# Performance work log

Hardware: AMD Instinct MI355X
Metric: run time of the kernel (lower is better)

The kernel has to match this reference:

```python
import jax, jax.numpy as jnp
import numpy as np

HIDDEN = 768
HEADS = 12
HEAD_DIM = HIDDEN // HEADS  # 64


def setup_inputs() -> dict:
    key = jax.random.key(0)
    k1, k2, k3 = jax.random.split(key, 3)
    B, N, C = 64, 197, HIDDEN
    hidden_states = jax.random.normal(k1, (B, N, C), dtype=jnp.float32)
    # qkv Linear: weight [C, 3C] (stored transposed for x @ W), bias [3C]
    w_qkv = jax.random.normal(k2, (C, 3 * C), dtype=jnp.float32) * (1.0 / np.sqrt(C))
    b_qkv = jax.random.normal(k3, (3 * C,), dtype=jnp.float32) * 0.02
    return {"hidden_states": hidden_states, "w_qkv": w_qkv, "b_qkv": b_qkv}


def reference(hidden_states, w_qkv, b_qkv):
    B, N, C = hidden_states.shape
    scale = HEAD_DIM ** -0.5
    qkv = hidden_states @ w_qkv + b_qkv                      # [B, N, 3C]
    qkv = qkv.reshape(B, N, 3, HEADS, HEAD_DIM)
    qkv = jnp.transpose(qkv, (2, 0, 3, 1, 4))                # [3, B, H, N, d]
    q, k, v = qkv[0], qkv[1], qkv[2]
    scores = jnp.einsum("bhqd,bhkd->bhqk", q, k) * scale     # [B, H, N, N]
    probs = jax.nn.softmax(scores, axis=-1)
    # dropout is identity in eval mode (p=0.0)
    ctx = jnp.einsum("bhqk,bhkd->bhqd", probs, v)            # [B, H, N, d]
    ctx = jnp.transpose(ctx, (0, 2, 1, 3)).reshape(B, N, C)  # [B, N, C]
    return ctx
```

## Files before the change

### kernel.cpp

```cpp
#include <hip/hip_runtime.h>

#define M_ROWS 12608
#define K_DIM  768
#define QSZ    9682944
#define XB_ELEMS 9732096

typedef __bf16 bf16x8 __attribute__((ext_vector_type(8)));
typedef float  f32x4  __attribute__((ext_vector_type(4)));

__device__ __forceinline__ unsigned short f2bf(float f) {
    unsigned u = __builtin_bit_cast(unsigned, f);
    u += 0x7fffu + ((u >> 16) & 1u);
    return (unsigned short)(u >> 16);
}

__device__ __forceinline__ void gll16(const unsigned short* g, unsigned short* l) {
    __builtin_amdgcn_global_load_lds(
        (const __attribute__((address_space(1))) unsigned int*)g,
        (__attribute__((address_space(3))) unsigned int*)l, 16, 0, 0);
}

__global__ void x2bf_kernel(const float* __restrict__ X, unsigned short* __restrict__ Xb) {
    size_t base = ((size_t)blockIdx.x * 256 + threadIdx.x) * 8;
    float4 a = *(const float4*)(X + base);
    float4 b = *(const float4*)(X + base + 4);
    ushort4 lo, hi;
    lo.x = f2bf(a.x); lo.y = f2bf(a.y); lo.z = f2bf(a.z); lo.w = f2bf(a.w);
    hi.x = f2bf(b.x); hi.y = f2bf(b.y); hi.z = f2bf(b.z); hi.w = f2bf(b.w);
    *(ushort4*)(Xb + base) = lo;
    *(ushort4*)(Xb + base + 4) = hi;
}

__global__ void wtrans_kernel(const float* __restrict__ W, unsigned short* __restrict__ Wt) {
    __shared__ float tile[32][33];
    int n0 = blockIdx.x * 32, k0 = blockIdx.y * 32;
    int tx = threadIdx.x, ty = threadIdx.y;
#pragma unroll
    for (int i = 0; i < 4; ++i)
        tile[ty + i * 8][tx] = W[(size_t)(k0 + ty + i * 8) * 2304 + n0 + tx];
    __syncthreads();
#pragma unroll
    for (int i = 0; i < 4; ++i)
        Wt[(size_t)(n0 + ty + i * 8) * K_DIM + k0 + tx] = f2bf(tile[tx][ty + i * 8]);
}

__global__ __launch_bounds__(256, 4) void qkv_gemm_kernel(
        const unsigned short* __restrict__ Xb, const unsigned short* __restrict__ Wt,
        const float* __restrict__ bias, unsigned short* __restrict__ qkv) {
    __shared__ __align__(16) unsigned short As[2][4096];
    __shared__ __align__(16) unsigned short Bs[2][4096];

    const int lin = blockIdx.x;
    const int xcd = lin & 7, ix = lin >> 3;
    const int wg = (xcd < 6) ? xcd * 223 + ix : 1338 + (xcd - 6) * 222 + ix;
    const int by = wg / 18, bx = wg - by * 18;
    const int m0 = by * 128, n0 = bx * 128;

    const int t = threadIdx.x;
    const int w = t >> 6, lane = t & 63, quad = lane >> 4, l16 = lane & 15;
    const int wr = (w >> 1) * 64, wc = (w & 1) * 64;

    const int s0 = w * 128 + lane;
    const int r0 = s0 & 127, kc0 = s0 >> 7;
    const int s1 = s0 + 64;
    const int r1 = s1 & 127, kc1 = s1 >> 7;
    const unsigned short* a0 = Xb + (size_t)(m0 + r0) * K_DIM + kc0 * 8;
    const unsigned short* a1 = Xb + (size_t)(m0 + r1) * K_DIM + kc1 * 8;
    const unsigned short* b0 = Wt + (size_t)(n0 + r0) * K_DIM + kc0 * 8;
    const unsigned short* b1 = Wt + (size_t)(n0 + r1) * K_DIM + kc1 * 8;

    f32x4 acc[4][4];
#pragma unroll
    for (int i = 0; i < 4; ++i)
#pragma unroll
        for (int j = 0; j < 4; ++j) acc[i][j] = (f32x4){0.f, 0.f, 0.f, 0.f};

    gll16(a0, &As[0][w * 1024]);
    gll16(a1, &As[0][w * 1024 + 512]);
    gll16(b0, &Bs[0][w * 1024]);
    gll16(b1, &Bs[0][w * 1024 + 512]);
    asm volatile("s_waitcnt vmcnt(0)" ::: "memory");
    __builtin_amdgcn_s_barrier();
    asm volatile("" ::: "memory");

#pragma unroll 2
    for (int kt = 0; kt < 24; ++kt) {
        const int cur = kt & 1, nxt = cur ^ 1;
        const int sk = (kt + 1 < 24 ? kt + 1 : 0) * 32;

        gll16(a0 + sk, &As[nxt][w * 1024]);
        gll16(a1 + sk, &As[nxt][w * 1024 + 512]);
        gll16(b0 + sk, &Bs[nxt][w * 1024]);
        gll16(b1 + sk, &Bs[nxt][w * 1024 + 512]);

        bf16x8 af[4], bfr[4];
#pragma unroll
        for (int i = 0; i < 4; ++i)
            af[i] = *(const bf16x8*)&As[cur][quad * 1024 + (wr + i * 16 + l16) * 8];
#pragma unroll
        for (int j = 0; j < 4; ++j)
            bfr[j] = *(const bf16x8*)&Bs[cur][quad * 1024 + (wc + j * 16 + l16) * 8];

#pragma unroll
        for (int i = 0; i < 4; ++i)
#pragma unroll
            for (int j = 0; j < 4; ++j)
                acc[i][j] = __builtin_amdgcn_mfma_f32_16x16x32_bf16(af[i], bfr[j], acc[i][j], 0, 0, 0);

        asm volatile("s_waitcnt vmcnt(0)" ::: "memory");
        __builtin_amdgcn_s_barrier();
        asm volatile("" ::: "memory");
    }

#pragma unroll
    for (int i = 0; i < 4; ++i) {
#pragma unroll
        for (int j = 0; j < 4; ++j) {
            int gn = n0 + wc + j * 16 + l16;
            int which = gn / 768;
            int rem = gn - which * 768;
            int hh = rem >> 6, dd = rem & 63;
            float bv = bias[gn];
#pragma unroll
            for (int r = 0; r < 4; ++r) {
                int gm = m0 + wr + i * 16 + quad * 4 + r;
                if (gm >= M_ROWS) continue;
                int bb = gm / 197;
                int tok = gm - bb * 197;
                float val = acc[i][j][r] + bv;
                if (which == 0) val *= 0.125f;
                size_t dst = (size_t)which * QSZ +
                             ((size_t)((bb * 12 + hh) * 197 + tok) * 64 + dd);
                qkv[dst] = f2bf(val);
            }
        }
    }
}

__global__ __launch_bounds__(256, 2) void attn_kernel(
        const unsigned short* __restrict__ qkv, float* __restrict__ out) {
    __shared__ __align__(16) unsigned short Ks[197 * 72];
    __shared__ __align__(16) unsigned short Vt[64 * 216];
    __shared__ __align__(16) unsigned short Ps[4 * 16 * 136];

    const int g = blockIdx.x;
    const int b = g / 12, h = g - b * 12;
    const int t = threadIdx.x, w = t >> 6, lane = t & 63;
    const int quad = lane >> 4, l16 = lane & 15;

    const size_t headoff = (size_t)(g * 197) * 64;
    const unsigned short* Qg = qkv + headoff;
    const unsigned short* Kg = qkv + (size_t)QSZ + headoff;
    const unsigned short* Vg = qkv + (size_t)2 * QSZ + headoff;

    for (int idx = t; idx < 1576; idx += 256) {
        int row = idx >> 3, c8 = (idx & 7) * 8;
        *(uint4*)&Ks[row * 72 + c8] = *(const uint4*)(Kg + (size_t)row * 64 + c8);
    }
    for (int idx = t; idx < 64 * 19; idx += 256) {
        int d = idx / 19, c = 197 + idx - d * 19;
        Vt[d * 216 + c] = 0;
    }
    for (int idx = t; idx < 1576; idx += 256) {
        int tok = idx >> 3, d0 = (idx & 7) * 8;
        ushort4 v0 = *(const ushort4*)(Vg + (size_t)tok * 64 + d0);
        ushort4 v1 = *(const ushort4*)(Vg + (size_t)tok * 64 + d0 + 4);
        Vt[(d0 + 0) * 216 + tok] = v0.x;
        Vt[(d0 + 1) * 216 + tok] = v0.y;
        Vt[(d0 + 2) * 216 + tok] = v0.z;
        Vt[(d0 + 3) * 216 + tok] = v0.w;
        Vt[(d0 + 4) * 216 + tok] = v1.x;
        Vt[(d0 + 5) * 216 + tok] = v1.y;
        Vt[(d0 + 6) * 216 + tok] = v1.z;
        Vt[(d0 + 7) * 216 + tok] = v1.w;
    }
    __syncthreads();

    unsigned short* Pw = Ps + w * (16 * 136);

    for (int tile = w; tile < 13; tile += 4) {
        int rq = tile * 16 + l16;
        int tokq = rq < 197 ? rq : 196;
        bf16x8 aq0 = *(const bf16x8*)(Qg + (size_t)tokq * 64 + quad * 8);
        bf16x8 aq1 = *(const bf16x8*)(Qg + (size_t)tokq * 64 + 32 + quad * 8);

        f32x4 s[13];
#pragma unroll
        for (int c = 0; c < 13; ++c) {
            int krow = c * 16 + l16;
            if (krow > 196) krow = 196;
            bf16x8 kb0 = *(const bf16x8*)&Ks[krow * 72 + quad * 8];
            bf16x8 kb1 = *(const bf16x8*)&Ks[krow * 72 + 32 + quad * 8];
            f32x4 zz = (f32x4){0.f, 0.f, 0.f, 0.f};
            zz = __builtin_amdgcn_mfma_f32_16x16x32_bf16(aq0, kb0, zz, 0, 0, 0);
            zz = __builtin_amdgcn_mfma_f32_16x16x32_bf16(aq1, kb1, zz, 0, 0, 0);
            s[c] = zz;
        }
        if (l16 >= 5) { s[12][0] = -1e30f; s[12][1] = -1e30f; s[12][2] = -1e30f; s[12][3] = -1e30f; }

        float mx[4], lsum[4];
#pragma unroll
        for (int r = 0; r < 4; ++r) {
            float m = s[0][r];
#pragma unroll
            for (int c = 1; c < 13; ++c) m = fmaxf(m, s[c][r]);
#pragma unroll
            for (int d = 1; d < 16; d <<= 1) m = fmaxf(m, __shfl_xor(m, d));
            mx[r] = m;
            lsum[r] = 0.f;
        }
#pragma unroll
        for (int c = 0; c < 13; ++c)
#pragma unroll
            for (int r = 0; r < 4; ++r) {
                float p = __expf(s[c][r] - mx[r]);
                s[c][r] = p;
                lsum[r] += p;
            }
#pragma unroll
        for (int r = 0; r < 4; ++r)
#pragma unroll
            for (int d = 1; d < 16; d <<= 1) lsum[r] += __shfl_xor(lsum[r], d);

        f32x4 o[4];
#pragma unroll
        for (int j = 0; j < 4; ++j) o[j] = (f32x4){0.f, 0.f, 0.f, 0.f};

#pragma unroll
        for (int c = 0; c < 8; ++c)
#pragma unroll
            for (int r = 0; r < 4; ++r)
                Pw[(quad * 4 + r) * 136 + c * 16 + l16] = f2bf(s[c][r]);
#pragma unroll
        for (int kc = 0; kc < 4; ++kc) {
            int kof = kc * 32 + quad * 8;
            bf16x8 ap = *(const bf16x8*)&Pw[l16 * 136 + kof];
#pragma unroll
            for (int j = 0; j < 4; ++j) {
                bf16x8 bv = *(const bf16x8*)&Vt[(j * 16 + l16) * 216 + kof];
                o[j] = __builtin_amdgcn_mfma_f32_16x16x32_bf16(ap, bv, o[j], 0, 0, 0);
            }
        }
#pragma unroll
        for (int r = 0; r < 4; ++r)
            Pw[(quad * 4 + r) * 136 + 80 + l16] = 0;
#pragma unroll
        for (int c = 8; c < 13; ++c)
#pragma unroll
            for (int r = 0; r < 4; ++r)
                Pw[(quad * 4 + r) * 136 + (c - 8) * 16 + l16] = f2bf(s[c][r]);
#pragma unroll
        for (int kc = 0; kc < 3; ++kc) {
            int kofA = kc * 32 + quad * 8;
            int kofB = (kc == 2 && quad >= 2) ? 0 : kofA;
            bf16x8 ap = *(const bf16x8*)&Pw[l16 * 136 + kofA];
#pragma unroll
            for (int j = 0; j < 4; ++j) {
                bf16x8 bv = *(const bf16x8*)&Vt[(j * 16 + l16) * 216 + 128 + kofB];
                o[j] = __builtin_amdgcn_mfma_f32_16x16x32_bf16(ap, bv, o[j], 0, 0, 0);
            }
        }

        int tokbase = tile * 16 + quad * 4;
#pragma unroll
        for (int r = 0; r < 4; ++r) {
            int tr = tokbase + r;
            if (tr >= 197) continue;
            float inv = 1.f / lsum[r];
#pragma unroll
            for (int j = 0; j < 4; ++j)
                out[((size_t)(b * 197 + tr)) * 768 + h * 64 + j * 16 + l16] = o[j][r] * inv;
        }
    }
}

extern "C" void kernel_launch(void* const* d_in, const int* in_sizes, int n_in,
                              void* d_out, int out_size, void* d_ws, size_t ws_size,
                              hipStream_t stream) {
    const float* X    = (const float*)d_in[0];
    const float* W    = (const float*)d_in[1];
    const float* bias = (const float*)d_in[2];
    unsigned short* ws = (unsigned short*)d_ws;
    float* out = (float*)d_out;

    unsigned short* Xb = (unsigned short*)d_out;
    unsigned short* Wt = (unsigned short*)d_out + XB_ELEMS;

    x2bf_kernel<<<4728, 256, 0, stream>>>(X, Xb);
    wtrans_kernel<<<dim3(72, 24), dim3(32, 8), 0, stream>>>(W, Wt);
    qkv_gemm_kernel<<<1782, 256, 0, stream>>>(Xb, Wt, bias, ws);
    attn_kernel<<<768, 256, 0, stream>>>(ws, out);
}
```

Baseline: 228.0 us.

## Fuse prep kernels, split QKV GEMM launch, add MFMA priority hints in attention

Merges the X-to-bf16 conversion and weight transpose into one prep kernel to save a launch. Splits the QKV GEMM grid into two launches using a block offset, which keeps the tile mapping but changes dispatch order across XCDs. Adds s_setprio around the MFMA loops in the attention kernel so those waves get issue priority while others do softmax. The extra GEMM launch and the disturbed XCD placement could offset the savings.

```diff
diff --git a/kernel.cpp b/kernel.cpp
--- a/kernel.cpp
+++ b/kernel.cpp
@@ -20,21 +20,25 @@
         (__attribute__((address_space(3))) unsigned int*)l, 16, 0, 0);
 }
 
-__global__ void x2bf_kernel(const float* __restrict__ X, unsigned short* __restrict__ Xb) {
-    size_t base = ((size_t)blockIdx.x * 256 + threadIdx.x) * 8;
-    float4 a = *(const float4*)(X + base);
-    float4 b = *(const float4*)(X + base + 4);
-    ushort4 lo, hi;
-    lo.x = f2bf(a.x); lo.y = f2bf(a.y); lo.z = f2bf(a.z); lo.w = f2bf(a.w);
-    hi.x = f2bf(b.x); hi.y = f2bf(b.y); hi.z = f2bf(b.z); hi.w = f2bf(b.w);
-    *(ushort4*)(Xb + base) = lo;
-    *(ushort4*)(Xb + base + 4) = hi;
-}
-
-__global__ void wtrans_kernel(const float* __restrict__ W, unsigned short* __restrict__ Wt) {
+__global__ __launch_bounds__(256) void prep_kernel(
+        const float* __restrict__ X, unsigned short* __restrict__ Xb,
+        const float* __restrict__ W, unsigned short* __restrict__ Wt) {
     __shared__ float tile[32][33];
-    int n0 = blockIdx.x * 32, k0 = blockIdx.y * 32;
-    int tx = threadIdx.x, ty = threadIdx.y;
+    const int bid = blockIdx.x;
+    if (bid < 4728) {
+        size_t base = ((size_t)bid * 256 + threadIdx.x) * 8;
+        float4 a = *(const float4*)(X + base);
+        float4 b = *(const float4*)(X + base + 4);
+        ushort4 lo, hi;
+        lo.x = f2bf(a.x); lo.y = f2bf(a.y); lo.z = f2bf(a.z); lo.w = f2bf(a.w);
+        hi.x = f2bf(b.x); hi.y = f2bf(b.y); hi.z = f2bf(b.z); hi.w = f2bf(b.w);
+        *(ushort4*)(Xb + base) = lo;
+        *(ushort4*)(Xb + base + 4) = hi;
+        return;
+    }
+    const int b2 = bid - 4728;
+    const int n0 = (b2 % 72) * 32, k0 = (b2 / 72) * 32;
+    const int tx = threadIdx.x & 31, ty = threadIdx.x >> 5;
 #pragma unroll
     for (int i = 0; i < 4; ++i)
         tile[ty + i * 8][tx] = W[(size_t)(k0 + ty + i * 8) * 2304 + n0 + tx];
@@ -46,11 +50,12 @@
 
 __global__ __launch_bounds__(256, 4) void qkv_gemm_kernel(
         const unsigned short* __restrict__ Xb, const unsigned short* __restrict__ Wt,
-        const float* __restrict__ bias, unsigned short* __restrict__ qkv) {
+        const float* __restrict__ bias, unsigned short* __restrict__ qkv,
+        const int loff) {
     __shared__ __align__(16) unsigned short As[2][4096];
     __shared__ __align__(16) unsigned short Bs[2][4096];
 
-    const int lin = blockIdx.x;
+    const int lin = blockIdx.x + loff;
     const int xcd = lin & 7, ix = lin >> 3;
     const int wg = (xcd < 6) ? xcd * 223 + ix : 1338 + (xcd - 6) * 222 + ix;
     const int by = wg / 18, bx = wg - by * 18;
@@ -185,6 +190,7 @@
         bf16x8 aq1 = *(const bf16x8*)(Qg + (size_t)tokq * 64 + 32 + quad * 8);
 
         f32x4 s[13];
+        __builtin_amdgcn_s_setprio(1);
 #pragma unroll
         for (int c = 0; c < 13; ++c) {
             int krow = c * 16 + l16;
@@ -196,6 +202,7 @@
             zz = __builtin_amdgcn_mfma_f32_16x16x32_bf16(aq1, kb1, zz, 0, 0, 0);
             s[c] = zz;
         }
+        __builtin_amdgcn_s_setprio(0);
         if (l16 >= 5) { s[12][0] = -1e30f; s[12][1] = -1e30f; s[12][2] = -1e30f; s[12][3] = -1e30f; }
 
         float mx[4], lsum[4];
@@ -231,6 +238,7 @@
 #pragma unroll
             for (int r = 0; r < 4; ++r)
                 Pw[(quad * 4 + r) * 136 + c * 16 + l16] = f2bf(s[c][r]);
+        __builtin_amdgcn_s_setprio(1);
 #pragma unroll
         for (int kc = 0; kc < 4; ++kc) {
             int kof = kc * 32 + quad * 8;
@@ -241,6 +249,7 @@
                 o[j] = __builtin_amdgcn_mfma_f32_16x16x32_bf16(ap, bv, o[j], 0, 0, 0);
             }
         }
+        __builtin_amdgcn_s_setprio(0);
 #pragma unroll
         for (int r = 0; r < 4; ++r)
             Pw[(quad * 4 + r) * 136 + 80 + l16] = 0;
@@ -249,6 +258,7 @@
 #pragma unroll
             for (int r = 0; r < 4; ++r)
                 Pw[(quad * 4 + r) * 136 + (c - 8) * 16 + l16] = f2bf(s[c][r]);
+        __builtin_amdgcn_s_setprio(1);
 #pragma unroll
         for (int kc = 0; kc < 3; ++kc) {
             int kofA = kc * 32 + quad * 8;
@@ -260,6 +270,7 @@
                 o[j] = __builtin_amdgcn_mfma_f32_16x16x32_bf16(ap, bv, o[j], 0, 0, 0);
             }
         }
+        __builtin_amdgcn_s_setprio(0);
 
         int tokbase = tile * 16 + quad * 4;
 #pragma unroll
@@ -286,8 +297,8 @@
     unsigned short* Xb = (unsigned short*)d_out;
     unsigned short* Wt = (unsigned short*)d_out + XB_ELEMS;
 
-    x2bf_kernel<<<4728, 256, 0, stream>>>(X, Xb);
-    wtrans_kernel<<<dim3(72, 24), dim3(32, 8), 0, stream>>>(W, Wt);
-    qkv_gemm_kernel<<<1782, 256, 0, stream>>>(Xb, Wt, bias, ws);
+    prep_kernel<<<6456, 256, 0, stream>>>(X, Xb, W, Wt);
+    qkv_gemm_kernel<<<891, 256, 0, stream>>>(Xb, Wt, bias, ws, 0);
+    qkv_gemm_kernel<<<891, 256, 0, stream>>>(Xb, Wt, bias, ws, 891);
     attn_kernel<<<768, 256, 0, stream>>>(ws, out);
 }
```

New measurement: 248.2 us. 8.9% more time.
